# Kernel optimization log

Hardware: AMD Instinct MI355X
Metric: run time of the kernel (lower is better)

## Reference

```python
import jax, jax.numpy as jnp
import numpy as np

H = 16  # n_heads

def setup_inputs() -> dict:
    key = jax.random.key(0)
    k1, k2, k3, k4 = jax.random.split(key, 4)
    B, S, D = 2, 2048, 1024
    query = jax.random.normal(k1, (B, S, D), dtype=jnp.float32)
    pos_emb = jax.random.normal(k2, (S, D), dtype=jnp.float32)
    w_qkv = jax.random.normal(k3, (D, 3 * D), dtype=jnp.float32) * (D ** -0.5)
    w_out = jax.random.normal(k4, (D, D), dtype=jnp.float32) * (D ** -0.5)
    return {"query": query, "pos_emb": pos_emb, "w_qkv": w_qkv, "w_out": w_out}

def reference(query, pos_emb, w_qkv, w_out):
    B, S, D = query.shape
    d_k = D // H
    # ape=True: pos_fn applied to input before QKV projection (additive APE)
    x = query + pos_emb[None, :, :]
    # fused QKV projection; torch view(B,S,H,3*d_k) + chunk(3,-1) == reshape(B,S,H,3,d_k)
    qkv = jnp.einsum('bsd,de->bse', x, w_qkv).reshape(B, S, H, 3, d_k)
    qkv = jnp.transpose(qkv, (0, 2, 1, 3, 4))  # [B,H,S,3,d_k]
    q, k, v = qkv[..., 0, :], qkv[..., 1, :], qkv[..., 2, :]
    scale = d_k ** -0.5
    scores = jnp.einsum('bhqd,bhkd->bhqk', q, k) * scale  # [B,H,S,S]
    attn = jax.nn.softmax(scores, axis=-1)  # dropout is identity in eval
    o = jnp.einsum('bhqk,bhkd->bhqd', attn, v)
    o = jnp.transpose(o, (0, 2, 1, 3)).reshape(B, S, D)
    return jnp.einsum('bsd,de->bse', o, w_out)
```

## Files before the change

kernel.cpp:

```cpp
#include <hip/hip_runtime.h>

#define SS 2048
#define DD 1024
#define N3 3072

typedef unsigned short u16;
typedef unsigned int u32;
typedef __attribute__((ext_vector_type(8))) short bf16x8;
typedef __attribute__((ext_vector_type(4))) float f32x4;

__device__ __forceinline__ u16 f2bf(float f) {
    u32 u = __float_as_uint(f);
    u32 r = u + 0x7fffu + ((u >> 16) & 1u);
    return (u16)(r >> 16);
}

__device__ __forceinline__ float fast_exp2(float x) {
    return __builtin_amdgcn_exp2f(x);
}

__device__ __forceinline__ void async_cp16(u16* lds, const u16* g) {
    __builtin_amdgcn_global_load_lds((const __attribute__((address_space(1))) u32*)g,
                                     (__attribute__((address_space(3))) u32*)lds, 16, 0, 0);
}

__global__ __launch_bounds__(256)
void prep_x(const float* __restrict__ q, const float* __restrict__ pos, u16* __restrict__ x)
{
    const size_t i = ((size_t)blockIdx.x * 256 + threadIdx.x) * 4;
    float4 a = *(const float4*)(q + i);
    float4 p = *(const float4*)(pos + (i & (size_t)(SS * DD - 1)));
    uint2 r;
    r.x = (u32)f2bf(a.x + p.x) | ((u32)f2bf(a.y + p.y) << 16);
    r.y = (u32)f2bf(a.z + p.z) | ((u32)f2bf(a.w + p.w) << 16);
    *(uint2*)(x + i) = r;
}

__global__ __launch_bounds__(256)
void transpose_bf16(const float* __restrict__ W, u16* __restrict__ WT, int K, int N)
{
    __shared__ float t[32][33];
    const int tx = threadIdx.x & 31, ty = threadIdx.x >> 5;
    const int x0 = blockIdx.x * 32, y0 = blockIdx.y * 32;
#pragma unroll
    for (int i = 0; i < 4; ++i)
        t[ty + i * 8][tx] = W[(size_t)(y0 + ty + i * 8) * N + x0 + tx];
    __syncthreads();
#pragma unroll
    for (int i = 0; i < 4; ++i)
        WT[(size_t)(x0 + ty + i * 8) * K + y0 + tx] = f2bf(t[tx][ty + i * 8]);
}

template <int OUT_BF16, int NT>
__global__ __launch_bounds__(256)
void gemm_mfma(const u16* __restrict__ A, const u16* __restrict__ BT,
               void* __restrict__ Cv, int M, int N, int K)
{
    constexpr int FR = NT / 32;
    __shared__ u16 As[128 * 64];
    __shared__ u16 Bs[NT * 64];

    const int tid = threadIdx.x;
    const int lane = tid & 63, wv = tid >> 6;
    const int quad = lane >> 4, l16 = lane & 15;
    const int m0 = blockIdx.y * 128, n0 = blockIdx.x * NT;

    const int arow = wv * 32 + (lane >> 3);
    const int pc   = lane & 7;
    const int lcA  = pc ^ (arow & 7);
    const u16* agp = A + (size_t)(m0 + arow) * K + lcA * 8;
    u16* alp = As + arow * 64 + pc * 8;

    const int brow = (NT == 128) ? (wv * 32 + (lane >> 3)) : (wv * 8 + (lane >> 3));
    const int lcB  = pc ^ (brow & 7);
    const u16* bgp = BT + (size_t)(n0 + brow) * K + lcB * 8;
    u16* blp = Bs + brow * 64 + pc * 8;

    const int moff = (wv >> 1) * 64, noff = (wv & 1) * (NT / 2);

    f32x4 acc[4][FR];
#pragma unroll
    for (int i = 0; i < 4; ++i)
#pragma unroll
        for (int j = 0; j < FR; ++j) acc[i][j] = {0.f, 0.f, 0.f, 0.f};

    const int swf = l16 & 7;

    for (int k0 = 0; k0 < K; k0 += 64) {
#pragma unroll
        for (int s = 0; s < 4; ++s)
            async_cp16(alp + s * 8 * 64, agp + (size_t)(s * 8) * K + k0);
        if constexpr (NT == 128) {
#pragma unroll
            for (int s = 0; s < 4; ++s)
                async_cp16(blp + s * 8 * 64, bgp + (size_t)(s * 8) * K + k0);
        } else {
#pragma unroll
            for (int s = 0; s < 2; ++s)
                async_cp16(blp + s * 32 * 64, bgp + (size_t)(s * 32) * K + k0);
        }
        __syncthreads();

#pragma unroll
        for (int ks = 0; ks < 2; ++ks) {
            bf16x8 af[4], bfr[FR];
#pragma unroll
            for (int t = 0; t < 4; ++t)
                af[t] = *(const bf16x8*)&As[(moff + t * 16 + l16) * 64 + (((ks * 4 + quad) ^ swf) << 3)];
#pragma unroll
            for (int t = 0; t < FR; ++t)
                bfr[t] = *(const bf16x8*)&Bs[(noff + t * 16 + l16) * 64 + (((ks * 4 + quad) ^ swf) << 3)];
#pragma unroll
            for (int mt = 0; mt < 4; ++mt)
#pragma unroll
                for (int nt = 0; nt < FR; ++nt)
                    acc[mt][nt] = __builtin_amdgcn_mfma_f32_16x16x32_bf16(af[mt], bfr[nt], acc[mt][nt], 0, 0, 0);
        }
        __syncthreads();
    }

#pragma unroll
    for (int mt = 0; mt < 4; ++mt)
#pragma unroll
        for (int r = 0; r < 4; ++r) {
            const size_t row = m0 + moff + mt * 16 + quad * 4 + r;
            if (OUT_BF16) {
                u16* cp = (u16*)Cv + row * N + n0 + noff + l16;
#pragma unroll
                for (int nt = 0; nt < FR; ++nt) cp[nt * 16] = f2bf(acc[mt][nt][r]);
            } else {
                float* cp = (float*)Cv + row * N + n0 + noff + l16;
#pragma unroll
                for (int nt = 0; nt < FR; ++nt) cp[nt * 16] = acc[mt][nt][r];
            }
        }
}

__global__ __launch_bounds__(256)
void attn_mfma(const u16* __restrict__ qkv, u16* __restrict__ o)
{
    __shared__ u16 Ks[64 * 64];
    __shared__ u16 Vn[64 * 64];
    __shared__ u16 Vt[64 * 64];
    __shared__ u16 Ps[4][32 * 64];

    const int tid = threadIdx.x;
    const int lane = tid & 63, wv = tid >> 6;
    const int quad = lane >> 4, l16 = lane & 15;
    const int bx = blockIdx.x;
    const int h = bx & 15, b = (bx >> 4) & 1, qt = bx >> 5;

    const size_t hb = (size_t)b * SS * N3 + h * 192;
    const int q0 = qt * 128 + wv * 32;
    const int sw = l16 & 7;

    bf16x8 qf[2][2];
#pragma unroll
    for (int mt = 0; mt < 2; ++mt)
#pragma unroll
        for (int ks = 0; ks < 2; ++ks)
            qf[mt][ks] = *(const bf16x8*)(qkv + hb + (size_t)(q0 + mt * 16 + l16) * N3 + ks * 32 + quad * 8);

    f32x4 po[2][4];
#pragma unroll
    for (int mt = 0; mt < 2; ++mt)
#pragma unroll
        for (int nt = 0; nt < 4; ++nt) po[mt][nt] = {0.f, 0.f, 0.f, 0.f};
    float lrun[2] = {0.f, 0.f};

    const int skey = tid >> 2;
    const int sc16 = (tid & 3) * 16;
    const int c0 = (tid & 3) * 2;
    const u16* kg = qkv + hb + 64 + (size_t)skey * N3 + sc16;
    const u16* vg = kg + 64;
    const int ksw = skey & 7;
    u16* kst0 = &Ks[skey * 64 + (((c0    ) ^ ksw) << 3)];
    u16* kst1 = &Ks[skey * 64 + (((c0 + 1) ^ ksw) << 3)];
    u16* vst0 = &Vn[skey * 64 + (((c0    ) ^ ksw) << 3)];
    u16* vst1 = &Vn[skey * 64 + (((c0 + 1) ^ ksw) << 3)];

    const int kp = tid & 31, dkb = (tid >> 5) * 8;

    const float CEXP = 0.125f * 1.44269504f;

    for (int kt = 0; kt < SS / 64; ++kt) {
        const size_t koff = (size_t)kt * 64 * N3;
        uint4 kv0 = *(const uint4*)(kg + koff);
        uint4 kv1 = *(const uint4*)(kg + koff + 8);
        uint4 vv0 = *(const uint4*)(vg + koff);
        uint4 vv1 = *(const uint4*)(vg + koff + 8);
        *(uint4*)kst0 = kv0;  *(uint4*)kst1 = kv1;
        *(uint4*)vst0 = vv0;  *(uint4*)vst1 = vv1;
        __syncthreads();

        {
            uint4 a4 = *(const uint4*)&Vn[(2 * kp)     * 64 + (((dkb >> 3) ^ ((2 * kp)     & 7)) << 3)];
            uint4 b4 = *(const uint4*)&Vn[(2 * kp + 1) * 64 + (((dkb >> 3) ^ ((2 * kp + 1) & 7)) << 3)];
            u32 ar[4] = {a4.x, a4.y, a4.z, a4.w};
            u32 br[4] = {b4.x, b4.y, b4.z, b4.w};
#pragma unroll
            for (int j = 0; j < 8; ++j) {
                const u32 sel = (j & 1) ? 0x07060302u : 0x05040100u;
                const u32 w = __builtin_amdgcn_perm(br[j >> 1], ar[j >> 1], sel);
                const int row = dkb + j;
                *(u32*)&Vt[row * 64 + (((kp >> 2) ^ (row & 7)) << 3) + ((2 * kp) & 7)] = w;
            }
        }

        f32x4 sf[2][4];
#pragma unroll
        for (int mt = 0; mt < 2; ++mt)
#pragma unroll
            for (int kn = 0; kn < 4; ++kn) sf[mt][kn] = {0.f, 0.f, 0.f, 0.f};
#pragma unroll
        for (int ks = 0; ks < 2; ++ks)
#pragma unroll
            for (int kn = 0; kn < 4; ++kn) {
                bf16x8 kf = *(const bf16x8*)&Ks[(kn * 16 + l16) * 64 + (((ks * 4 + quad) ^ sw) << 3)];
#pragma unroll
                for (int mt = 0; mt < 2; ++mt)
                    sf[mt][kn] = __builtin_amdgcn_mfma_f32_16x16x32_bf16(kf, qf[mt][ks], sf[mt][kn], 0, 0, 0);
            }

#pragma unroll
        for (int mt = 0; mt < 2; ++mt) {
            float ls = 0.f;
#pragma unroll
            for (int kn = 0; kn < 4; ++kn) {
                const float p0 = fast_exp2(sf[mt][kn][0] * CEXP);
                const float p1 = fast_exp2(sf[mt][kn][1] * CEXP);
                const float p2 = fast_exp2(sf[mt][kn][2] * CEXP);
                const float p3 = fast_exp2(sf[mt][kn][3] * CEXP);
                const u32 w0 = __builtin_amdgcn_perm(__float_as_uint(p1), __float_as_uint(p0), 0x07060302u);
                const u32 w1 = __builtin_amdgcn_perm(__float_as_uint(p3), __float_as_uint(p2), 0x07060302u);
                ls += __uint_as_float(w0 << 16) + __uint_as_float(w0 & 0xffff0000u)
                    + __uint_as_float(w1 << 16) + __uint_as_float(w1 & 0xffff0000u);
                const int ch = (2 * kn + (quad >> 1)) ^ sw;
                uint2 wp; wp.x = w0; wp.y = w1;
                *(uint2*)&Ps[wv][(mt * 16 + l16) * 64 + (ch << 3) + ((quad & 1) << 2)] = wp;
            }
            lrun[mt] += ls;
        }
        __syncthreads();

#pragma unroll
        for (int ks = 0; ks < 2; ++ks) {
            bf16x8 pf[2], vf[4];
#pragma unroll
            for (int mt = 0; mt < 2; ++mt)
                pf[mt] = *(const bf16x8*)&Ps[wv][(mt * 16 + l16) * 64 + (((ks * 4 + quad) ^ sw) << 3)];
#pragma unroll
            for (int nt = 0; nt < 4; ++nt)
                vf[nt] = *(const bf16x8*)&Vt[(nt * 16 + l16) * 64 + (((ks * 4 + quad) ^ sw) << 3)];
#pragma unroll
            for (int mt = 0; mt < 2; ++mt)
#pragma unroll
                for (int nt = 0; nt < 4; ++nt)
                    po[mt][nt] = __builtin_amdgcn_mfma_f32_16x16x32_bf16(pf[mt], vf[nt], po[mt][nt], 0, 0, 0);
        }
        __syncthreads();
    }

#pragma unroll
    for (int mt = 0; mt < 2; ++mt) {
        lrun[mt] += __shfl_xor(lrun[mt], 16, 64);
        lrun[mt] += __shfl_xor(lrun[mt], 32, 64);
    }
#pragma unroll
    for (int mt = 0; mt < 2; ++mt) {
        float linv[4];
#pragma unroll
        for (int r = 0; r < 4; ++r)
            linv[r] = 1.f / __shfl(lrun[mt], quad * 4 + r, 64);
#pragma unroll
        for (int r = 0; r < 4; ++r) {
            const size_t row = (size_t)b * SS + q0 + mt * 16 + quad * 4 + r;
            u16* op = o + row * DD + h * 64 + l16;
#pragma unroll
            for (int nt = 0; nt < 4; ++nt)
                op[nt * 16] = f2bf(po[mt][nt][r] * linv[r]);
        }
    }
}

extern "C" void kernel_launch(void* const* d_in, const int* in_sizes, int n_in,
                              void* d_out, int out_size, void* d_ws, size_t ws_size,
                              hipStream_t stream)
{
    const float* query  = (const float*)d_in[0];
    const float* posemb = (const float*)d_in[1];
    const float* w_qkv  = (const float*)d_in[2];
    const float* w_out  = (const float*)d_in[3];
    float* out = (float*)d_out;

    u16* xb    = (u16*)d_ws;
    u16* wqkvT = xb    + (size_t)4096 * 1024;
    u16* woutT = wqkvT + (size_t)3072 * 1024;
    u16* qkv   = woutT + (size_t)1024 * 1024;
    u16* ob    = qkv   + (size_t)4096 * 3072;

    prep_x<<<4096, 256, 0, stream>>>(query, posemb, xb);
    transpose_bf16<<<dim3(N3 / 32, DD / 32), 256, 0, stream>>>(w_qkv, wqkvT, DD, N3);
    transpose_bf16<<<dim3(DD / 32, DD / 32), 256, 0, stream>>>(w_out, woutT, DD, DD);

    gemm_mfma<1, 128><<<dim3(N3 / 128, 4096 / 128), 256, 0, stream>>>(xb, wqkvT, (void*)qkv, 4096, N3, DD);

    attn_mfma<<<dim3(512, 1, 1), 256, 0, stream>>>(qkv, ob);

    gemm_mfma<0, 64><<<dim3(DD / 64, 4096 / 128), 256, 0, stream>>>(ob, woutT, (void*)out, 4096, DD, DD);
}
```

Measured before the change: 200.1 us.

## Double-buffer K/V with async LDS loads and fold softmax scale into Q weights

The attention kernel now double-buffers the K and V tiles in LDS. It prefetches the next tile with direct global-to-LDS async copies while computing on the current one, and replaces the `__syncthreads` calls with explicit waitcnt plus barrier sequences, dropping the trailing barrier. The softmax scale and log2(e) factor are folded into the Q columns of the QKV weight during the bf16 transpose, which removes a multiply per score. `s_setprio` is raised around the MFMA sections. The goal is to hide global load latency and cut barrier overhead, at the cost of more LDS and slightly different rounding of the scaled Q.

Measured after the change: 201.4 us. Within noise of the previous version (+0.6%).

```diff
diff --git a/kernel.cpp b/kernel.cpp
--- a/kernel.cpp
+++ b/kernel.cpp
@@ -36,6 +36,7 @@
     *(uint2*)(x + i) = r;
 }
 
+template <int SQ>
 __global__ __launch_bounds__(256)
 void transpose_bf16(const float* __restrict__ W, u16* __restrict__ WT, int K, int N)
 {
@@ -47,8 +48,12 @@
         t[ty + i * 8][tx] = W[(size_t)(y0 + ty + i * 8) * N + x0 + tx];
     __syncthreads();
 #pragma unroll
-    for (int i = 0; i < 4; ++i)
-        WT[(size_t)(x0 + ty + i * 8) * K + y0 + tx] = f2bf(t[tx][ty + i * 8]);
+    for (int i = 0; i < 4; ++i) {
+        const int n = x0 + ty + i * 8;
+        float v = t[tx][ty + i * 8];
+        if (SQ && (n % 192) < 64) v *= 0.18033688f;
+        WT[(size_t)n * K + y0 + tx] = f2bf(v);
+    }
 }
 
 template <int OUT_BF16, int NT>
@@ -139,8 +144,8 @@
 __global__ __launch_bounds__(256)
 void attn_mfma(const u16* __restrict__ qkv, u16* __restrict__ o)
 {
-    __shared__ u16 Ks[64 * 64];
-    __shared__ u16 Vn[64 * 64];
+    __shared__ u16 Ks[2][64 * 64];
+    __shared__ u16 Vn[2][64 * 64];
     __shared__ u16 Vt[64 * 64];
     __shared__ u16 Ps[4][32 * 64];
 
@@ -168,34 +173,46 @@
         for (int nt = 0; nt < 4; ++nt) po[mt][nt] = {0.f, 0.f, 0.f, 0.f};
     float lrun[2] = {0.f, 0.f};
 
-    const int skey = tid >> 2;
-    const int sc16 = (tid & 3) * 16;
-    const int c0 = (tid & 3) * 2;
-    const u16* kg = qkv + hb + 64 + (size_t)skey * N3 + sc16;
-    const u16* vg = kg + 64;
-    const int ksw = skey & 7;
-    u16* kst0 = &Ks[skey * 64 + (((c0    ) ^ ksw) << 3)];
-    u16* kst1 = &Ks[skey * 64 + (((c0 + 1) ^ ksw) << 3)];
-    u16* vst0 = &Vn[skey * 64 + (((c0    ) ^ ksw) << 3)];
-    u16* vst1 = &Vn[skey * 64 + (((c0 + 1) ^ ksw) << 3)];
+    const int lrow = lane >> 3;
+    const int pc8  = lane & 7;
+    const int lc   = pc8 ^ lrow;
+    const int srow = wv * 16;
+    const u16* kgp = qkv + hb + 64  + (size_t)(srow + lrow) * N3 + lc * 8;
+    const u16* vgp = kgp + 64;
 
     const int kp = tid & 31, dkb = (tid >> 5) * 8;
 
-    const float CEXP = 0.125f * 1.44269504f;
+    {
+        u16* kb = Ks[0] + (srow + lrow) * 64 + pc8 * 8;
+        u16* vb = Vn[0] + (srow + lrow) * 64 + pc8 * 8;
+        async_cp16(kb,          kgp);
+        async_cp16(kb + 8 * 64, kgp + (size_t)8 * N3);
+        async_cp16(vb,          vgp);
+        async_cp16(vb + 8 * 64, vgp + (size_t)8 * N3);
+    }
 
     for (int kt = 0; kt < SS / 64; ++kt) {
-        const size_t koff = (size_t)kt * 64 * N3;
-        uint4 kv0 = *(const uint4*)(kg + koff);
-        uint4 kv1 = *(const uint4*)(kg + koff + 8);
-        uint4 vv0 = *(const uint4*)(vg + koff);
-        uint4 vv1 = *(const uint4*)(vg + koff + 8);
-        *(uint4*)kst0 = kv0;  *(uint4*)kst1 = kv1;
-        *(uint4*)vst0 = vv0;  *(uint4*)vst1 = vv1;
-        __syncthreads();
+        const int p = kt & 1;
+
+        if (kt < SS / 64 - 1) {
+            const size_t koff = (size_t)(kt + 1) * 64 * N3;
+            u16* kb = Ks[p ^ 1] + (srow + lrow) * 64 + pc8 * 8;
+            u16* vb = Vn[p ^ 1] + (srow + lrow) * 64 + pc8 * 8;
+            async_cp16(kb,          kgp + koff);
+            async_cp16(kb + 8 * 64, kgp + koff + (size_t)8 * N3);
+            async_cp16(vb,          vgp + koff);
+            async_cp16(vb + 8 * 64, vgp + koff + (size_t)8 * N3);
+            asm volatile("s_waitcnt vmcnt(4) lgkmcnt(0)\n\ts_barrier" ::: "memory");
+        } else {
+            asm volatile("s_waitcnt vmcnt(0) lgkmcnt(0)\n\ts_barrier" ::: "memory");
+        }
+
+        const u16* kbuf = Ks[p];
+        const u16* vbuf = Vn[p];
 
         {
-            uint4 a4 = *(const uint4*)&Vn[(2 * kp)     * 64 + (((dkb >> 3) ^ ((2 * kp)     & 7)) << 3)];
-            uint4 b4 = *(const uint4*)&Vn[(2 * kp + 1) * 64 + (((dkb >> 3) ^ ((2 * kp + 1) & 7)) << 3)];
+            uint4 a4 = *(const uint4*)&vbuf[(2 * kp)     * 64 + (((dkb >> 3) ^ ((2 * kp)     & 7)) << 3)];
+            uint4 b4 = *(const uint4*)&vbuf[(2 * kp + 1) * 64 + (((dkb >> 3) ^ ((2 * kp + 1) & 7)) << 3)];
             u32 ar[4] = {a4.x, a4.y, a4.z, a4.w};
             u32 br[4] = {b4.x, b4.y, b4.z, b4.w};
 #pragma unroll
@@ -212,25 +229,27 @@
         for (int mt = 0; mt < 2; ++mt)
 #pragma unroll
             for (int kn = 0; kn < 4; ++kn) sf[mt][kn] = {0.f, 0.f, 0.f, 0.f};
+        __builtin_amdgcn_s_setprio(1);
 #pragma unroll
         for (int ks = 0; ks < 2; ++ks)
 #pragma unroll
             for (int kn = 0; kn < 4; ++kn) {
-                bf16x8 kf = *(const bf16x8*)&Ks[(kn * 16 + l16) * 64 + (((ks * 4 + quad) ^ sw) << 3)];
+                bf16x8 kf = *(const bf16x8*)&kbuf[(kn * 16 + l16) * 64 + (((ks * 4 + quad) ^ sw) << 3)];
 #pragma unroll
                 for (int mt = 0; mt < 2; ++mt)
                     sf[mt][kn] = __builtin_amdgcn_mfma_f32_16x16x32_bf16(kf, qf[mt][ks], sf[mt][kn], 0, 0, 0);
             }
+        __builtin_amdgcn_s_setprio(0);
 
 #pragma unroll
         for (int mt = 0; mt < 2; ++mt) {
             float ls = 0.f;
 #pragma unroll
             for (int kn = 0; kn < 4; ++kn) {
-                const float p0 = fast_exp2(sf[mt][kn][0] * CEXP);
-                const float p1 = fast_exp2(sf[mt][kn][1] * CEXP);
-                const float p2 = fast_exp2(sf[mt][kn][2] * CEXP);
-                const float p3 = fast_exp2(sf[mt][kn][3] * CEXP);
+                const float p0 = fast_exp2(sf[mt][kn][0]);
+                const float p1 = fast_exp2(sf[mt][kn][1]);
+                const float p2 = fast_exp2(sf[mt][kn][2]);
+                const float p3 = fast_exp2(sf[mt][kn][3]);
                 const u32 w0 = __builtin_amdgcn_perm(__float_as_uint(p1), __float_as_uint(p0), 0x07060302u);
                 const u32 w1 = __builtin_amdgcn_perm(__float_as_uint(p3), __float_as_uint(p2), 0x07060302u);
                 ls += __uint_as_float(w0 << 16) + __uint_as_float(w0 & 0xffff0000u)
@@ -241,8 +260,10 @@
             }
             lrun[mt] += ls;
         }
-        __syncthreads();
-
+
+        asm volatile("s_waitcnt lgkmcnt(0)\n\ts_barrier" ::: "memory");
+
+        __builtin_amdgcn_s_setprio(1);
 #pragma unroll
         for (int ks = 0; ks < 2; ++ks) {
             bf16x8 pf[2], vf[4];
@@ -258,7 +279,7 @@
                 for (int nt = 0; nt < 4; ++nt)
                     po[mt][nt] = __builtin_amdgcn_mfma_f32_16x16x32_bf16(pf[mt], vf[nt], po[mt][nt], 0, 0, 0);
         }
-        __syncthreads();
+        __builtin_amdgcn_s_setprio(0);
     }
 
 #pragma unroll
@@ -300,8 +321,8 @@
     u16* ob    = qkv   + (size_t)4096 * 3072;
 
     prep_x<<<4096, 256, 0, stream>>>(query, posemb, xb);
-    transpose_bf16<<<dim3(N3 / 32, DD / 32), 256, 0, stream>>>(w_qkv, wqkvT, DD, N3);
-    transpose_bf16<<<dim3(DD / 32, DD / 32), 256, 0, stream>>>(w_out, woutT, DD, DD);
+    transpose_bf16<1><<<dim3(N3 / 32, DD / 32), 256, 0, stream>>>(w_qkv, wqkvT, DD, N3);
+    transpose_bf16<0><<<dim3(DD / 32, DD / 32), 256, 0, stream>>>(w_out, woutT, DD, DD);
 
     gemm_mfma<1, 128><<<dim3(N3 / 128, 4096 / 128), 256, 0, stream>>>(xb, wqkvT, (void*)qkv, 4096, N3, DD);
 
```
